# Kernel optimization log

Hardware: AMD Instinct MI355X
Metric: run time of the kernel (lower is better)

Reference implementation:

```python
import jax, jax.numpy as jnp
import numpy as np

N, E, D, G, L = 50000, 400000, 64, 256, 4
VA, VB = 64, 8   # atom / bond feature vocab sizes
NUM_ATOM_FEATS, NUM_BOND_FEATS = 9, 3
MSG_EPS = 1e-7   # GENConv message epsilon
LN_EPS = 1e-5


def layernorm(x, g, b):
    mu = x.mean(-1, keepdims=True)
    var = x.var(-1, keepdims=True)
    return (x - mu) * jax.lax.rsqrt(var + LN_EPS) * g + b


def genconv(h, edge_emb, src, dst, W, b):
    # GENConv (aggr='softmax', t=1, mlp_layers=1):
    # msg = relu(x_j + e) + eps; per-dst per-feature softmax-weighted sum; mlp(x + m)
    msg = jax.nn.relu(h[src] + edge_emb) + MSG_EPS          # [E, D]
    mmax = jax.ops.segment_max(msg, dst, num_segments=N)    # [N, D]
    mmax = jnp.where(jnp.isfinite(mmax), mmax, 0.0)         # nodes with no in-edges
    ex = jnp.exp(msg - mmax[dst])
    denom = jax.ops.segment_sum(ex, dst, num_segments=N)
    alpha = ex / jnp.maximum(denom[dst], 1e-16)
    m = jax.ops.segment_sum(alpha * msg, dst, num_segments=N)  # [N, D]
    return (h + m) @ W + b


def setup_inputs():
    key = jax.random.key(0)
    ks = jax.random.split(key, 10)
    x = jax.random.randint(ks[0], (N, NUM_ATOM_FEATS), 0, VA)
    edge_index = jax.random.randint(ks[1], (2, E), 0, N)
    edge_attr = jax.random.randint(ks[2], (E, NUM_BOND_FEATS), 0, VB)
    batch = jnp.sort(jax.random.randint(ks[3], (N,), 0, G))
    s = 0.02
    w = 1.0 / np.sqrt(D).astype(np.float32)
    atom_emb = jax.random.normal(ks[4], (NUM_ATOM_FEATS, VA, D), jnp.float32) * s
    bond_emb = jax.random.normal(ks[5], (NUM_BOND_FEATS, VB, D), jnp.float32) * s
    gcn_W = jax.random.normal(ks[6], (L, D, D), jnp.float32) * w
    gcn_b = jnp.zeros((L, D), jnp.float32)
    norm_g = jnp.ones((L, D), jnp.float32)
    norm_b = jnp.zeros((L, D), jnp.float32)
    vn_emb = jnp.zeros((1, D), jnp.float32)  # constant-init virtualnode embedding
    vn_W1 = jax.random.normal(ks[7], (L - 1, D, D), jnp.float32) * w
    vn_b1 = jnp.zeros((L - 1, D), jnp.float32)
    vn_g1 = jnp.ones((L - 1, D), jnp.float32)
    vn_be1 = jnp.zeros((L - 1, D), jnp.float32)
    vn_W2 = jax.random.normal(ks[8], (L - 1, D, D), jnp.float32) * w
    vn_b2 = jnp.zeros((L - 1, D), jnp.float32)
    vn_g2 = jnp.ones((L - 1, D), jnp.float32)
    vn_be2 = jnp.zeros((L - 1, D), jnp.float32)
    return dict(x=x, edge_index=edge_index, edge_attr=edge_attr, batch=batch,
                atom_emb=atom_emb, bond_emb=bond_emb, gcn_W=gcn_W, gcn_b=gcn_b,
                norm_g=norm_g, norm_b=norm_b, vn_emb=vn_emb,
                vn_W1=vn_W1, vn_b1=vn_b1, vn_g1=vn_g1, vn_be1=vn_be1,
                vn_W2=vn_W2, vn_b2=vn_b2, vn_g2=vn_g2, vn_be2=vn_be2)


def reference(x, edge_index, edge_attr, batch, atom_emb, bond_emb, gcn_W, gcn_b,
              norm_g, norm_b, vn_emb, vn_W1, vn_b1, vn_g1, vn_be1,
              vn_W2, vn_b2, vn_g2, vn_be2):
    src, dst = edge_index[0], edge_index[1]
    # AtomEncoder / BondEncoder: sum of per-feature embedding lookups
    h = atom_emb[jnp.arange(NUM_ATOM_FEATS)[None, :], x].sum(1)          # [N, D]
    edge_emb = bond_emb[jnp.arange(NUM_BOND_FEATS)[None, :], edge_attr].sum(1)  # [E, D]
    vn = jnp.broadcast_to(vn_emb[0], (G, D))
    h = h + vn[batch]
    # block == 'res+' (eval mode: dropout is identity)
    h = genconv(h, edge_emb, src, dst, gcn_W[0], gcn_b[0])
    for l in range(1, L):
        h2 = jax.nn.relu(layernorm(h, norm_g[l - 1], norm_b[l - 1]))
        vt = jax.ops.segment_sum(h2, batch, num_segments=G) + vn         # global_add_pool
        vt = jax.nn.relu(layernorm(vt @ vn_W1[l - 1] + vn_b1[l - 1], vn_g1[l - 1], vn_be1[l - 1]))
        vn = jax.nn.relu(layernorm(vt @ vn_W2[l - 1] + vn_b2[l - 1], vn_g2[l - 1], vn_be2[l - 1]))
        h2 = h2 + vn[batch]
        h = genconv(h2, edge_emb, src, dst, gcn_W[l], gcn_b[l]) + h
    return layernorm(h, norm_g[L - 1], norm_b[L - 1])
```

## Files before the change

kernel.cpp:

```cpp
#include <hip/hip_runtime.h>
#include <hip/hip_bf16.h>

typedef __hip_bfloat16 bf16;

#define GNUM 256
#define LN_EPS 1e-5f
#define MSG_EPS 1e-7f

typedef float f4v __attribute__((ext_vector_type(4)));
typedef short s8v __attribute__((ext_vector_type(8)));
typedef __bf16 b8v __attribute__((ext_vector_type(8)));

template <typename V>
__device__ auto mfma_bf16_(V a, V b, f4v c, int)
    -> decltype(__builtin_amdgcn_mfma_f32_16x16x32_bf16(a, b, c, 0, 0, 0)) {
  return __builtin_amdgcn_mfma_f32_16x16x32_bf16(a, b, c, 0, 0, 0);
}
template <typename V>
__device__ f4v mfma_bf16_(V a, V b, f4v c, long) {
  return __builtin_amdgcn_mfma_f32_16x16x32_bf16(__builtin_bit_cast(s8v, a),
                                                 __builtin_bit_cast(s8v, b), c, 0, 0, 0);
}
__device__ __forceinline__ f4v mfma16(uint4 a, uint4 b, f4v c){
  return mfma_bf16_(__builtin_bit_cast(b8v, a), __builtin_bit_cast(b8v, b), c, 0);
}

__device__ __forceinline__ float bu2f(unsigned short u){
  unsigned v = ((unsigned)u) << 16; return __builtin_bit_cast(float, v);
}
__device__ __forceinline__ unsigned short f2bu(float f){
  unsigned u = __builtin_bit_cast(unsigned, f);
  return (unsigned short)((u + 0x7FFFu + ((u >> 16) & 1u)) >> 16);
}

__device__ __forceinline__ float wave_sum64(float v){
  #pragma unroll
  for (int off = 32; off > 0; off >>= 1) v += __shfl_xor(v, off, 64);
  return v;
}

struct Params15 {
  const void* src[15];
  int n[15];
  int off[15];
};

__global__ __launch_bounds__(256) void k_convert(Params15 P, int* __restrict__ flag,
                                                 float* __restrict__ dst,
                                                 int* __restrict__ counts, int nc){
  __shared__ int isf_sh;
  int tid = threadIdx.x;
  if (tid < 64){
    const unsigned short* u = (const unsigned short*)P.src[0];
    int bad = 0;
    for (int k = tid; k < 256; k += 64){
      unsigned short v = u[2*k];
      if (((v >> 7) & 0xFFu) >= 137u) bad = 1;
    }
    unsigned long long m = __ballot(bad);
    if (tid == 0) isf_sh = (m != 0ull) ? 1 : 0;
  }
  __syncthreads();
  bool isf = (isf_sh != 0);
  if (blockIdx.x == 0 && tid == 0) *flag = isf ? 1 : 0;
  for (int a = 0; a < 15; ++a){
    int n = P.n[a];
    float* d = dst + P.off[a];
    if (isf){
      const float* s = (const float*)P.src[a];
      for (int i = blockIdx.x*256 + tid; i < n; i += gridDim.x*256) d[i] = s[i];
    } else {
      const bf16* s = (const bf16*)P.src[a];
      for (int i = blockIdx.x*256 + tid; i < n; i += gridDim.x*256) d[i] = __bfloat162float(s[i]);
    }
  }
  for (int i = blockIdx.x*256 + tid; i < nc; i += gridDim.x*256) counts[i] = 0;
}

__global__ void k_count(const int* __restrict__ dst, int* __restrict__ counts, int E){
  int e = blockIdx.x*256 + threadIdx.x;
  if (e < E) atomicAdd(counts + dst[e], 1);
}

__global__ __launch_bounds__(256) void k_scan1(const int* __restrict__ counts,
                                               int* __restrict__ offs,
                                               int* __restrict__ btot, int n){
  __shared__ int wsum[4];
  int tid = threadIdx.x, w = tid >> 6, lane = tid & 63;
  int i = blockIdx.x*256 + tid;
  int v = (i < n) ? counts[i] : 0;
  int incl = v;
  #pragma unroll
  for (int off = 1; off < 64; off <<= 1){
    int t = __shfl_up(incl, off, 64);
    if (lane >= off) incl += t;
  }
  if (lane == 63) wsum[w] = incl;
  __syncthreads();
  int woff = 0;
  for (int k = 0; k < w; ++k) woff += wsum[k];
  int tot = incl + woff;
  if (i < n) offs[i+1] = tot;
  if (tid == 255) btot[blockIdx.x] = tot;
}

__global__ __launch_bounds__(256) void k_scan2(const int* __restrict__ btot,
                                               int* __restrict__ bexc, int nb){
  __shared__ int wsum[4];
  __shared__ int carry_sh;
  int tid = threadIdx.x, w = tid >> 6, lane = tid & 63;
  if (tid == 0) carry_sh = 0;
  __syncthreads();
  for (int base = 0; base < nb; base += 256){
    int i = base + tid;
    int v = (i < nb) ? btot[i] : 0;
    int incl = v;
    #pragma unroll
    for (int off = 1; off < 64; off <<= 1){
      int t = __shfl_up(incl, off, 64);
      if (lane >= off) incl += t;
    }
    if (lane == 63) wsum[w] = incl;
    __syncthreads();
    int carry = carry_sh;
    int woff = 0;
    for (int k = 0; k < w; ++k) woff += wsum[k];
    if (i < nb) bexc[i] = carry + woff + incl - v;
    __syncthreads();
    if (tid == 0) carry_sh = carry + wsum[0] + wsum[1] + wsum[2] + wsum[3];
    __syncthreads();
  }
}

__global__ void k_scan3(int* __restrict__ offs, int* __restrict__ cursor,
                        const int* __restrict__ bexc, int n){
  int i = blockIdx.x*256 + threadIdx.x;
  if (i == 0){ offs[0] = 0; cursor[0] = 0; }
  if (i < n){
    int v = offs[i+1] + bexc[blockIdx.x];
    offs[i+1] = v;
    if (i+1 < n) cursor[i+1] = v;
  }
}

__global__ void k_scatter(const int* __restrict__ src, const int* __restrict__ dst,
                          const int* __restrict__ ea, int* __restrict__ cursor,
                          int* __restrict__ payload, int E){
  int e = blockIdx.x*256 + threadIdx.x;
  if (e >= E) return;
  int d = dst[e];
  int pos = atomicAdd(cursor + d, 1);
  payload[pos] = (src[e] & 0xFFFF) | (ea[e*3] << 16) | (ea[e*3+1] << 19) | (ea[e*3+2] << 22);
}

__global__ void k_prep(const float* __restrict__ gw, unsigned short* __restrict__ Wf,
                       const int* __restrict__ batch, int* __restrict__ goffs,
                       const int* __restrict__ x, const float* __restrict__ atom_emb,
                       const float* __restrict__ vn_emb, unsigned short* __restrict__ b0,
                       int n){
  if (blockIdx.x < 64){
    int t = blockIdx.x*256 + threadIdx.x;
    int j = t & 7, lane = (t >> 3) & 63, nt = (t >> 9) & 3, kt = (t >> 11) & 1, l = t >> 12;
    int k = kt*32 + (lane >> 4)*8 + j;
    int c = nt*16 + (lane & 15);
    Wf[t] = f2bu(gw[l*4096 + k*64 + c]);
  } else if (blockIdx.x < 66){
    int g = (blockIdx.x - 64)*256 + threadIdx.x;
    if (g > GNUM) return;
    if (g == GNUM){ goffs[GNUM] = n; return; }
    int lo = 0, hi = n;
    while (lo < hi){ int mid = (lo+hi)>>1; if (batch[mid] < g) lo = mid+1; else hi = mid; }
    goffs[g] = lo;
  } else {
    int t = (blockIdx.x - 66) * 256 + threadIdx.x;
    int i = t >> 6, j = t & 63;
    if (i >= n) return;
    float acc = vn_emb[j];
    #pragma unroll
    for (int f = 0; f < 9; ++f){
      int idx = x[i*9 + f];
      acc += atom_emb[(f*64 + idx)*64 + j];
    }
    b0[t] = f2bu(acc);
  }
}

__global__ __launch_bounds__(1024) void k_agg_t(
    const unsigned short* __restrict__ b0, const int* __restrict__ offs,
    const int* __restrict__ payload, const float* __restrict__ bond,
    unsigned short* __restrict__ tbuf, int n){
  __shared__ float Bs[1536];
  int tid = threadIdx.x;
  for (int idx = tid; idx < 1536; idx += 1024) Bs[idx] = bond[idx];
  __syncthreads();
  int w = tid >> 6, j = tid & 63;
  int v = blockIdx.x * 16 + w;
  if (v >= n) return;
  int e0 = offs[v], e1 = offs[v+1];
  float own = bu2f(b0[(size_t)v*64 + j]);
  float tv;
  if (e1 > e0){
    float den = 0.f, num = 0.f;
    for (int e = e0; e < e1; e += 8){
      float m[8];
      #pragma unroll
      for (int u = 0; u < 8; ++u){
        int ei = e + u;
        bool valid = ei < e1;
        int idx = valid ? ei : e0;
        int p = payload[idx];
        int s = p & 0xFFFF;
        float eev = Bs[((p >> 16) & 7)*64 + j]
                  + Bs[(8 + ((p >> 19) & 7))*64 + j]
                  + Bs[(16 + ((p >> 22) & 7))*64 + j];
        float hv = bu2f(b0[(size_t)s*64 + j]);
        float mm = fmaxf(hv + eev, 0.f) + MSG_EPS;
        m[u] = valid ? mm : -100.f;
      }
      #pragma unroll
      for (int u = 0; u < 8; ++u){
        float ex = __expf(m[u]);
        den += ex;
        num += ex * m[u];
      }
    }
    tv = own + num / fmaxf(den, 1e-16f);
  } else {
    tv = own;
  }
  tbuf[(size_t)v*64 + j] = f2bu(tv);
}

__global__ __launch_bounds__(256) void k_gemm_ln(
    const unsigned short* __restrict__ tbuf, const unsigned short* __restrict__ Wf,
    const float* __restrict__ bias, float* __restrict__ hres,
    unsigned short* __restrict__ h2b, void* __restrict__ finalout,
    const float* __restrict__ ng, const float* __restrict__ nb,
    const int* __restrict__ flag, int use_res, int mode, int n){
  int tid = threadIdx.x;
  int w = tid >> 6, lane = tid & 63;
  int quad = lane >> 4, lm = lane & 15;
  int v0 = blockIdx.x * 64;
  uint4 Bfr[2][4];
  const uint4* Wfv = (const uint4*)Wf;
  #pragma unroll
  for (int kt = 0; kt < 2; ++kt)
    #pragma unroll
    for (int nt = 0; nt < 4; ++nt)
      Bfr[kt][nt] = Wfv[(size_t)((kt*4 + nt)*64 + lane)];
  int arow = v0 + w*16 + lm;
  const uint4* tg = (const uint4*)tbuf;
  uint4 A0 = tg[(size_t)arow*8 + quad];
  uint4 A1 = tg[(size_t)arow*8 + 4 + quad];
  f4v acc[4];
  #pragma unroll
  for (int nt = 0; nt < 4; ++nt) acc[nt] = (f4v){0.f,0.f,0.f,0.f};
  #pragma unroll
  for (int nt = 0; nt < 4; ++nt) acc[nt] = mfma16(A0, Bfr[0][nt], acc[nt]);
  #pragma unroll
  for (int nt = 0; nt < 4; ++nt) acc[nt] = mfma16(A1, Bfr[1][nt], acc[nt]);
  float s1[4] = {0,0,0,0}, s2[4] = {0,0,0,0};
  #pragma unroll
  for (int nt = 0; nt < 4; ++nt){
    int col = nt*16 + lm;
    float bv = bias[col];
    #pragma unroll
    for (int reg = 0; reg < 4; ++reg){
      int row = v0 + w*16 + quad*4 + reg;
      float val = acc[nt][reg] + bv;
      if (use_res && row < n) val += hres[(size_t)row*64 + col];
      acc[nt][reg] = val;
      s1[reg] += val;
      s2[reg] += val*val;
    }
  }
  #pragma unroll
  for (int reg = 0; reg < 4; ++reg){
    #pragma unroll
    for (int m = 1; m < 16; m <<= 1){
      s1[reg] += __shfl_xor(s1[reg], m, 64);
      s2[reg] += __shfl_xor(s2[reg], m, 64);
    }
  }
  bool isf = (mode == 1) && (*flag != 0);
  #pragma unroll
  for (int reg = 0; reg < 4; ++reg){
    int row = v0 + w*16 + quad*4 + reg;
    if (row >= n) continue;
    float mu = s1[reg] * (1.f/64.f);
    float var = fmaxf(s2[reg] * (1.f/64.f) - mu*mu, 0.f);
    float rstd = rsqrtf(var + LN_EPS);
    #pragma unroll
    for (int nt = 0; nt < 4; ++nt){
      int col = nt*16 + lm;
      float val = acc[nt][reg];
      float y = (val - mu) * rstd * ng[col] + nb[col];
      size_t o = (size_t)row*64 + col;
      if (mode == 0){
        hres[o] = val;
        h2b[o] = f2bu(fmaxf(y, 0.f));
      } else {
        if (isf) ((float*)finalout)[o] = y;
        else     ((bf16*)finalout)[o]  = __float2bfloat16(y);
      }
    }
  }
}

__global__ __launch_bounds__(256) void k_vn(
    const unsigned short* __restrict__ h2b, const int* __restrict__ goffs,
    const float* __restrict__ vn_emb, float* __restrict__ vn,
    unsigned short* __restrict__ b0,
    const float* __restrict__ W1, const float* __restrict__ b1,
    const float* __restrict__ g1, const float* __restrict__ be1,
    const float* __restrict__ W2, const float* __restrict__ b2,
    const float* __restrict__ g2, const float* __restrict__ be2,
    int first){
  __shared__ float Ws[4096];
  __shared__ float part[4][64];
  __shared__ float rowbuf[64];
  __shared__ float vnew[64];
  int tid = threadIdx.x, w = tid >> 6, j = tid & 63, g = blockIdx.x;
  for (int idx = tid; idx < 4096; idx += 256) Ws[idx] = W1[idx];
  int r0 = goffs[g], r1 = goffs[g+1];
  float sum = 0.f;
  for (int i = r0 + w; i < r1; i += 4) sum += bu2f(h2b[(size_t)i*64 + j]);
  part[w][j] = sum;
  __syncthreads();
  float y = 0.f;
  if (tid < 64){
    float s = part[0][j] + part[1][j] + part[2][j] + part[3][j]
            + (first ? vn_emb[j] : vn[(size_t)g*64 + j]);
    rowbuf[j] = s;
  }
  __syncthreads();
  if (tid < 64){
    float acc = b1[j];
    #pragma unroll
    for (int k = 0; k < 64; ++k) acc = fmaf(rowbuf[k], Ws[k*64 + j], acc);
    float mu = wave_sum64(acc) * (1.f/64.f);
    float d = acc - mu;
    float var = wave_sum64(d*d) * (1.f/64.f);
    y = fmaxf(d * rsqrtf(var + LN_EPS) * g1[j] + be1[j], 0.f);
  }
  __syncthreads();
  for (int idx = tid; idx < 4096; idx += 256) Ws[idx] = W2[idx];
  if (tid < 64) rowbuf[j] = y;
  __syncthreads();
  if (tid < 64){
    float acc = b2[j];
    #pragma unroll
    for (int k = 0; k < 64; ++k) acc = fmaf(rowbuf[k], Ws[k*64 + j], acc);
    float mu = wave_sum64(acc) * (1.f/64.f);
    float d = acc - mu;
    float var = wave_sum64(d*d) * (1.f/64.f);
    float v2 = fmaxf(d * rsqrtf(var + LN_EPS) * g2[j] + be2[j], 0.f);
    vn[(size_t)g*64 + j] = v2;
    vnew[j] = v2;
  }
  __syncthreads();
  float vj = vnew[j];
  for (int i = r0 + w; i < r1; i += 4)
    b0[(size_t)i*64 + j] = f2bu(bu2f(h2b[(size_t)i*64 + j]) + vj);
}

extern "C" void kernel_launch(void* const* d_in, const int* in_sizes, int n_in,
                              void* d_out, int out_size, void* d_ws, size_t ws_size,
                              hipStream_t stream){
  const int* x          = (const int*)d_in[0];
  const int* edge_index = (const int*)d_in[1];
  const int* edge_attr  = (const int*)d_in[2];
  const int* batch      = (const int*)d_in[3];

  const int N = in_sizes[3];
  const int E = in_sizes[2] / 3;
  const int L = 4;

  const int P_ATOM = 0, P_BOND = 36864, P_GW = 38400, P_GB = 54784,
            P_NG = 55040, P_NB = 55296, P_VNE = 55552, P_W1 = 55616,
            P_B1 = 67904, P_G1 = 68096, P_BE1 = 68288, P_W2 = 68480,
            P_B2 = 80768, P_G2 = 80960, P_BE2 = 81152, P_END = 81344;

  char* ws = (char*)d_ws;
  size_t off = 0;
  auto alloc = [&](size_t bytes)->char*{
    char* p = ws + off; off += (bytes + 255) & ~(size_t)255; return p;
  };
  int*    flag   = (int*)alloc(256);
  float*  par    = (float*)alloc((size_t)P_END * 4);
  unsigned short* Wf  = (unsigned short*)alloc(16384 * 2);
  unsigned short* b0  = (unsigned short*)alloc((size_t)N*64*2);
  unsigned short* tb  = (unsigned short*)alloc((size_t)(N+64)*64*2);
  unsigned short* h2b = (unsigned short*)alloc((size_t)N*64*2);
  float*  h      = (float*)alloc((size_t)N*64*4);
  int*    counts = (int*)alloc((size_t)N*4);
  int*    offs   = (int*)alloc((size_t)(N+1)*4);
  int*    cursor = (int*)alloc((size_t)N*4);
  int*    btot   = (int*)alloc(1024);
  int*    bexc   = (int*)alloc(1024);
  int*    payload= (int*)alloc((size_t)E*4);
  int*    goffs  = (int*)alloc((size_t)(GNUM+1)*4);
  float*  vn     = (float*)alloc((size_t)GNUM*64*4);
  (void)ws_size; (void)n_in; (void)out_size;

  Params15 P;
  const int poffs[15] = {P_ATOM,P_BOND,P_GW,P_GB,P_NG,P_NB,P_VNE,P_W1,P_B1,P_G1,P_BE1,P_W2,P_B2,P_G2,P_BE2};
  for (int a = 0; a < 15; ++a){ P.src[a] = d_in[4+a]; P.n[a] = in_sizes[4+a]; P.off[a] = poffs[a]; }

  int nodeGrid = (N*64 + 255) / 256;
  int nScanB   = (N + 255) / 256;
  int eGrid    = (E + 255) / 256;
  const int* srcp = edge_index;
  const int* dstp = edge_index + E;

  k_convert<<<128, 256, 0, stream>>>(P, flag, par, counts, N);
  k_count<<<eGrid, 256, 0, stream>>>(dstp, counts, E);
  k_scan1<<<nScanB, 256, 0, stream>>>(counts, offs, btot, N);
  k_scan2<<<1, 256, 0, stream>>>(btot, bexc, nScanB);
  k_scan3<<<nScanB, 256, 0, stream>>>(offs, cursor, bexc, N);
  k_scatter<<<eGrid, 256, 0, stream>>>(srcp, dstp, edge_attr, cursor, payload, E);
  k_prep<<<66 + nodeGrid, 256, 0, stream>>>(par + P_GW, Wf, batch, goffs,
                                            x, par + P_ATOM, par + P_VNE, b0, N);

  int gemmGrid = (N + 63) / 64;
  int aggGrid  = (N + 15) / 16;
  for (int l = 0; l < L; ++l){
    if (l > 0){
      k_vn<<<GNUM, 256, 0, stream>>>(h2b, goffs, par + P_VNE, vn, b0,
                                     par + P_W1 + (l-1)*4096, par + P_B1 + (l-1)*64,
                                     par + P_G1 + (l-1)*64, par + P_BE1 + (l-1)*64,
                                     par + P_W2 + (l-1)*4096, par + P_B2 + (l-1)*64,
                                     par + P_G2 + (l-1)*64, par + P_BE2 + (l-1)*64,
                                     l == 1 ? 1 : 0);
    }
    k_agg_t<<<aggGrid, 1024, 0, stream>>>(b0, offs, payload, par + P_BOND, tb, N);
    int mode = (l == L-1) ? 1 : 0;
    k_gemm_ln<<<gemmGrid, 256, 0, stream>>>(tb, Wf + (size_t)l*4096,
                                            par + P_GB + l*64, h, h2b, d_out,
                                            par + P_NG + l*64, par + P_NB + l*64,
                                            flag, l > 0 ? 1 : 0, mode, N);
  }
}
```

Measured before the change: 414.3 us.

## Fuse edge softmax aggregation with GEMM+LayerNorm into one per-layer kernel

Merges the per-node softmax aggregation kernel and the MFMA GEMM+LayerNorm kernel into a single kernel. Each wavefront aggregates 16 nodes in sequence, stages the bf16 results in shared memory and feeds them straight into the MFMA. This removes the global tbuf round trip and one launch per layer. Offsets are loaded once per wave and broadcast via shuffle. In exchange, each wave now handles 16 nodes serially instead of 16 waves per block each taking one node, which lowers parallelism in the latency-bound gather phase and could worsen load imbalance.

```diff
diff --git a/kernel.cpp b/kernel.cpp
--- a/kernel.cpp
+++ b/kernel.cpp
@@ -185,62 +185,66 @@
   }
 }
 
-__global__ __launch_bounds__(1024) void k_agg_t(
+__global__ __launch_bounds__(256) void k_layer(
     const unsigned short* __restrict__ b0, const int* __restrict__ offs,
     const int* __restrict__ payload, const float* __restrict__ bond,
-    unsigned short* __restrict__ tbuf, int n){
+    const unsigned short* __restrict__ Wf, const float* __restrict__ bias,
+    float* __restrict__ hres, unsigned short* __restrict__ h2b,
+    void* __restrict__ finalout, const float* __restrict__ ng,
+    const float* __restrict__ nb, const int* __restrict__ flag,
+    int use_res, int mode, int n){
   __shared__ float Bs[1536];
+  __shared__ __align__(16) unsigned short T[4][16][72];
   int tid = threadIdx.x;
-  for (int idx = tid; idx < 1536; idx += 1024) Bs[idx] = bond[idx];
+  for (int idx = tid; idx < 1536; idx += 256) Bs[idx] = bond[idx];
   __syncthreads();
   int w = tid >> 6, j = tid & 63;
-  int v = blockIdx.x * 16 + w;
-  if (v >= n) return;
-  int e0 = offs[v], e1 = offs[v+1];
-  float own = bu2f(b0[(size_t)v*64 + j]);
-  float tv;
-  if (e1 > e0){
-    float den = 0.f, num = 0.f;
-    for (int e = e0; e < e1; e += 8){
-      float m[8];
-      #pragma unroll
-      for (int u = 0; u < 8; ++u){
-        int ei = e + u;
-        bool valid = ei < e1;
-        int idx = valid ? ei : e0;
-        int p = payload[idx];
-        int s = p & 0xFFFF;
-        float eev = Bs[((p >> 16) & 7)*64 + j]
-                  + Bs[(8 + ((p >> 19) & 7))*64 + j]
-                  + Bs[(16 + ((p >> 22) & 7))*64 + j];
-        float hv = bu2f(b0[(size_t)s*64 + j]);
-        float mm = fmaxf(hv + eev, 0.f) + MSG_EPS;
-        m[u] = valid ? mm : -100.f;
+  int v0 = blockIdx.x * 64;
+  int vb = v0 + w*16;
+
+  int oidx = vb + (j < 17 ? j : 16);
+  if (oidx > n) oidx = n;
+  int o17 = offs[oidx];
+
+  for (int r = 0; r < 16; ++r){
+    int v = vb + r;
+    float tv = 0.f;
+    if (v < n){
+      int e0 = __builtin_amdgcn_readfirstlane(__shfl(o17, r, 64));
+      int e1 = __builtin_amdgcn_readfirstlane(__shfl(o17, r + 1, 64));
+      float own = bu2f(b0[(size_t)v*64 + j]);
+      tv = own;
+      if (e1 > e0){
+        float den = 0.f, num = 0.f;
+        for (int e = e0; e < e1; e += 8){
+          float m[8];
+          #pragma unroll
+          for (int u = 0; u < 8; ++u){
+            int ei = e + u;
+            bool valid = ei < e1;
+            int p = payload[valid ? ei : e0];
+            int s = p & 0xFFFF;
+            float eev = Bs[((p >> 16) & 7)*64 + j]
+                      + Bs[(8 + ((p >> 19) & 7))*64 + j]
+                      + Bs[(16 + ((p >> 22) & 7))*64 + j];
+            float hv = bu2f(b0[(size_t)s*64 + j]);
+            float mm = fmaxf(hv + eev, 0.f) + MSG_EPS;
+            m[u] = valid ? mm : -100.f;
+          }
+          #pragma unroll
+          for (int u = 0; u < 8; ++u){
+            float ex = __expf(m[u]);
+            den += ex;
+            num += ex * m[u];
+          }
+        }
+        tv = own + num / fmaxf(den, 1e-16f);
       }
-      #pragma unroll
-      for (int u = 0; u < 8; ++u){
-        float ex = __expf(m[u]);
-        den += ex;
-        num += ex * m[u];
-      }
-    }
-    tv = own + num / fmaxf(den, 1e-16f);
-  } else {
-    tv = own;
-  }
-  tbuf[(size_t)v*64 + j] = f2bu(tv);
-}
-
-__global__ __launch_bounds__(256) void k_gemm_ln(
-    const unsigned short* __restrict__ tbuf, const unsigned short* __restrict__ Wf,
-    const float* __restrict__ bias, float* __restrict__ hres,
-    unsigned short* __restrict__ h2b, void* __restrict__ finalout,
-    const float* __restrict__ ng, const float* __restrict__ nb,
-    const int* __restrict__ flag, int use_res, int mode, int n){
-  int tid = threadIdx.x;
-  int w = tid >> 6, lane = tid & 63;
-  int quad = lane >> 4, lm = lane & 15;
-  int v0 = blockIdx.x * 64;
+    }
+    T[w][r][j] = f2bu(tv);
+  }
+
+  int lane = j, quad = lane >> 4, lm = lane & 15;
   uint4 Bfr[2][4];
   const uint4* Wfv = (const uint4*)Wf;
   #pragma unroll
@@ -248,10 +252,8 @@
     #pragma unroll
     for (int nt = 0; nt < 4; ++nt)
       Bfr[kt][nt] = Wfv[(size_t)((kt*4 + nt)*64 + lane)];
-  int arow = v0 + w*16 + lm;
-  const uint4* tg = (const uint4*)tbuf;
-  uint4 A0 = tg[(size_t)arow*8 + quad];
-  uint4 A1 = tg[(size_t)arow*8 + 4 + quad];
+  uint4 A0 = *(const uint4*)&T[w][lm][8*quad];
+  uint4 A1 = *(const uint4*)&T[w][lm][32 + 8*quad];
   f4v acc[4];
   #pragma unroll
   for (int nt = 0; nt < 4; ++nt) acc[nt] = (f4v){0.f,0.f,0.f,0.f};
@@ -266,7 +268,7 @@
     float bv = bias[col];
     #pragma unroll
     for (int reg = 0; reg < 4; ++reg){
-      int row = v0 + w*16 + quad*4 + reg;
+      int row = vb + quad*4 + reg;
       float val = acc[nt][reg] + bv;
       if (use_res && row < n) val += hres[(size_t)row*64 + col];
       acc[nt][reg] = val;
@@ -285,7 +287,7 @@
   bool isf = (mode == 1) && (*flag != 0);
   #pragma unroll
   for (int reg = 0; reg < 4; ++reg){
-    int row = v0 + w*16 + quad*4 + reg;
+    int row = vb + quad*4 + reg;
     if (row >= n) continue;
     float mu = s1[reg] * (1.f/64.f);
     float var = fmaxf(s2[reg] * (1.f/64.f) - mu*mu, 0.f);
@@ -390,7 +392,6 @@
   float*  par    = (float*)alloc((size_t)P_END * 4);
   unsigned short* Wf  = (unsigned short*)alloc(16384 * 2);
   unsigned short* b0  = (unsigned short*)alloc((size_t)N*64*2);
-  unsigned short* tb  = (unsigned short*)alloc((size_t)(N+64)*64*2);
   unsigned short* h2b = (unsigned short*)alloc((size_t)N*64*2);
   float*  h      = (float*)alloc((size_t)N*64*4);
   int*    counts = (int*)alloc((size_t)N*4);
@@ -422,8 +423,7 @@
   k_prep<<<66 + nodeGrid, 256, 0, stream>>>(par + P_GW, Wf, batch, goffs,
                                             x, par + P_ATOM, par + P_VNE, b0, N);
 
-  int gemmGrid = (N + 63) / 64;
-  int aggGrid  = (N + 15) / 16;
+  int layerGrid = (N + 63) / 64;
   for (int l = 0; l < L; ++l){
     if (l > 0){
       k_vn<<<GNUM, 256, 0, stream>>>(h2b, goffs, par + P_VNE, vn, b0,
@@ -433,11 +433,11 @@
                                      par + P_G2 + (l-1)*64, par + P_BE2 + (l-1)*64,
                                      l == 1 ? 1 : 0);
     }
-    k_agg_t<<<aggGrid, 1024, 0, stream>>>(b0, offs, payload, par + P_BOND, tb, N);
     int mode = (l == L-1) ? 1 : 0;
-    k_gemm_ln<<<gemmGrid, 256, 0, stream>>>(tb, Wf + (size_t)l*4096,
-                                            par + P_GB + l*64, h, h2b, d_out,
-                                            par + P_NG + l*64, par + P_NB + l*64,
-                                            flag, l > 0 ? 1 : 0, mode, N);
-  }
-}
+    k_layer<<<layerGrid, 256, 0, stream>>>(b0, offs, payload, par + P_BOND,
+                                           Wf + (size_t)l*4096, par + P_GB + l*64,
+                                           h, h2b, d_out,
+                                           par + P_NG + l*64, par + P_NB + l*64,
+                                           flag, l > 0 ? 1 : 0, mode, N);
+  }
+}
```

New measurement: 449.1 us. +8.4%, slower.
